# Kernel optimization log

Hardware: AMD Instinct MI355X
Metric: run time of the kernel (lower is better)

## Reference

```python
import jax, jax.numpy as jnp
import numpy as np

N_NODES = 100000


def gcn_conv(x, W, b, src, dst, num_nodes):
    # PyG GCNConv: add self-loops, symmetric normalization, x @ W, scatter-add, + b
    xw = x @ W  # [N, out]
    loop = jnp.arange(num_nodes, dtype=src.dtype)
    s = jnp.concatenate([src, loop])  # message source j
    d = jnp.concatenate([dst, loop])  # aggregation target i
    deg = jax.ops.segment_sum(jnp.ones_like(d, dtype=xw.dtype), d, num_segments=num_nodes)
    dis = jnp.where(deg > 0, jax.lax.rsqrt(deg), 0.0)  # D^{-1/2}
    norm = dis[s] * dis[d]  # [E+N]
    msg = norm[:, None] * xw[s]  # gather + scale
    out = jax.ops.segment_sum(msg, d, num_segments=num_nodes)  # scatter-add
    return out + b


def setup_inputs() -> dict:
    key = jax.random.key(0)
    k1, k2, k3, k4 = jax.random.split(key, 4)
    F, H, E = 64, 64, 1250000
    x = jax.random.normal(k1, (N_NODES, F), dtype=jnp.float32)
    edge_index = jax.random.randint(k2, (2, E), 0, N_NODES, dtype=jnp.int64)
    W1 = jax.random.normal(k3, (F, H), dtype=jnp.float32) * (1.0 / np.sqrt(F))
    b1 = jnp.zeros((H,), dtype=jnp.float32)
    W2 = jax.random.normal(k4, (H, F), dtype=jnp.float32) * (1.0 / np.sqrt(H))
    b2 = jnp.zeros((F,), dtype=jnp.float32)
    return {"x": x, "edge_index": edge_index, "W1": W1, "b1": b1, "W2": W2, "b2": b2}


def reference(x, edge_index, W1, b1, W2, b2):
    src, dst = edge_index[0], edge_index[1]
    h = gcn_conv(x, W1, b1, src, dst, N_NODES)
    h = jax.nn.relu(h)
    out = gcn_conv(h, W2, b2, src, dst, N_NODES)
    return out
```

## Files before the change

### kernel.cpp

```cpp
#include <hip/hip_runtime.h>

#define NN    100000
#define F     64
#define NBUCK 391
#define CAPB  4096
#define TILE  4096
#define NBLKG 782
#define G1A   400

#define O_CURSOR 0
#define O_ROWPTR 512
#define O_DEG    100864
#define O_DIS    201216
#define O_PACKED 301568
#define O_SRT    1903104
#define O_AH     3504768
#define O_BH     6704768
#define O_W2F    9904768

typedef __attribute__((ext_vector_type(8))) short bf16x8;
typedef __attribute__((ext_vector_type(4))) float f32x4;
typedef __attribute__((ext_vector_type(2))) float f32x2;

__device__ __forceinline__ unsigned bf_rne(float x) {
    unsigned u = __float_as_uint(x);
    return (u + 0x7FFFu + ((u >> 16) & 1u)) >> 16;
}
__device__ __forceinline__ unsigned pack2(float lo, float hi) {
    return bf_rne(lo) | (bf_rne(hi) << 16);
}
__device__ __forceinline__ float lo_f(unsigned u) { return __uint_as_float(u << 16); }
__device__ __forceinline__ float hi_f(unsigned u) { return __uint_as_float(u & 0xFFFF0000u); }
__device__ __forceinline__ f32x2 up2(unsigned u) {
    f32x2 r = {__uint_as_float(u << 16), __uint_as_float(u & 0xFFFF0000u)};
    return r;
}

struct BpSmem {
    int hist[NBUCK], lofs[NBUCK], gbase[NBUCK], lcur[NBUCK];
    int wsum[8];
    unsigned stage[TILE];
    unsigned short sbuck[TILE];
};
union KSmem {
    BpSmem bp;
    unsigned w1f[16][64][4];
};
struct NsSmem {
    int h[256], lcur[256], wsum[4], ptot;
    int stage[CAPB];
};
union K2Smem {
    NsSmem ns;
    unsigned w1f[16][64][4];
};
struct K3Smem {
    unsigned w2f[16][64][4];
    unsigned hbuf[16 * 32];
    float dis_s[16];
};

__device__ __forceinline__ void binpack_body(const int* __restrict__ src,
                                             const int* __restrict__ dst, int E,
                                             int* __restrict__ cursor,
                                             unsigned* __restrict__ packed,
                                             int bid, BpSmem& sm) {
    int t  = threadIdx.x;
    int t0 = bid * TILE;
    int n  = min(TILE, E - t0);

    if (t < NBUCK) sm.hist[t] = 0;
    __syncthreads();
    int d_r[8], s_r[8];
#pragma unroll
    for (int it = 0; it < 8; ++it) {
        int i = t + it * 512;
        if (i < n) {
            d_r[it] = dst[t0 + i];
            s_r[it] = src[t0 + i];
            atomicAdd(&sm.hist[d_r[it] >> 8], 1);
        }
    }
    __syncthreads();
    int lane = t & 63, w = t >> 6;
    int v = (t < NBUCK) ? sm.hist[t] : 0;
    int s = v;
#pragma unroll
    for (int off = 1; off < 64; off <<= 1) {
        int u = __shfl_up(s, off, 64);
        if (lane >= off) s += u;
    }
    if (lane == 63) sm.wsum[w] = s;
    __syncthreads();
    if (t == 0) {
        int run = 0;
#pragma unroll
        for (int i = 0; i < 8; ++i) { int c = sm.wsum[i]; sm.wsum[i] = run; run += c; }
    }
    __syncthreads();
    if (t < NBUCK) {
        int ex = s - v + sm.wsum[w];
        sm.lofs[t] = ex;
        sm.lcur[t] = ex;
        sm.gbase[t] = t * CAPB + (v ? atomicAdd(&cursor[t], v) : 0);
    }
    __syncthreads();
#pragma unroll
    for (int it = 0; it < 8; ++it) {
        int i = t + it * 512;
        if (i < n) {
            int d = d_r[it];
            int b = d >> 8;
            int p = atomicAdd(&sm.lcur[b], 1);
            sm.stage[p] = ((unsigned)s_r[it] << 8) | (unsigned)(d & 255);
            sm.sbuck[p] = (unsigned short)b;
        }
    }
    __syncthreads();
    for (int i = t; i < n; i += 512) {
        int b = sm.sbuck[i];
        packed[sm.gbase[b] + (i - sm.lofs[b])] = sm.stage[i];
    }
}

__device__ __forceinline__ void gemm_mfma_body(const float* __restrict__ X,
                                               const float* __restrict__ W,
                                               unsigned* __restrict__ Ah, int bid,
                                               unsigned (*w1f)[64][4]) {
    int t = threadIdx.x;
    for (int idx = t; idx < 4096; idx += 512) {
        int slot = idx >> 8;
        int ks   = (slot >> 1) & 1;
        int p    = slot & 1;
        int ct   = slot >> 2;
        int l    = (idx >> 2) & 63;
        int j    = idx & 3;
        int k    = 32 * ks + 8 * (l >> 4) + 2 * j;
        int col  = 16 * ct + (l & 15);
        float v0 = W[k * 64 + col];
        float v1 = W[(k + 1) * 64 + col];
        if (p) {
            v0 -= __uint_as_float(bf_rne(v0) << 16);
            v1 -= __uint_as_float(bf_rne(v1) << 16);
        }
        ((unsigned*)w1f)[idx] = pack2(v0, v1);
    }

    int lane = t & 63, wid = t >> 6;
    int g = lane >> 4;
    int wrow0 = bid * 128 + wid * 16;
    int wrow  = wrow0 + (lane & 15);
    bool valid = wrow < NN;
    const float* xp = X + (size_t)wrow * F + 8 * g;
    float4 fz = {0.f, 0.f, 0.f, 0.f};
    float4 f0 = valid ? *(const float4*)(xp)      : fz;
    float4 f1 = valid ? *(const float4*)(xp + 4)  : fz;
    float4 f2 = valid ? *(const float4*)(xp + 32) : fz;
    float4 f3 = valid ? *(const float4*)(xp + 36) : fz;
    __syncthreads();

    f32x4 ac0 = {0.f,0.f,0.f,0.f}, ac1 = ac0, ac2 = ac0, ac3 = ac0;
#pragma unroll
    for (int ks = 0; ks < 2; ++ks) {
        float4 u0 = ks ? f2 : f0;
        float4 u1 = ks ? f3 : f1;
        uint4 hw;
        hw.x = pack2(u0.x, u0.y);
        hw.y = pack2(u0.z, u0.w);
        hw.z = pack2(u1.x, u1.y);
        hw.w = pack2(u1.z, u1.w);
        uint4 lw;
        lw.x = pack2(u0.x - lo_f(hw.x), u0.y - hi_f(hw.x));
        lw.y = pack2(u0.z - lo_f(hw.y), u0.w - hi_f(hw.y));
        lw.z = pack2(u1.x - lo_f(hw.z), u1.y - hi_f(hw.z));
        lw.w = pack2(u1.z - lo_f(hw.w), u1.w - hi_f(hw.w));
        bf16x8 Ahi = __builtin_bit_cast(bf16x8, hw);
        bf16x8 Alo = __builtin_bit_cast(bf16x8, lw);
#pragma unroll
        for (int ct = 0; ct < 4; ++ct) {
            uint4 bh = *(const uint4*)&w1f[ct * 4 + ks * 2 + 0][lane][0];
            uint4 bl = *(const uint4*)&w1f[ct * 4 + ks * 2 + 1][lane][0];
            bf16x8 Bh_ = __builtin_bit_cast(bf16x8, bh);
            bf16x8 Bl_ = __builtin_bit_cast(bf16x8, bl);
            f32x4& ac = (ct == 0) ? ac0 : (ct == 1) ? ac1 : (ct == 2) ? ac2 : ac3;
            ac = __builtin_amdgcn_mfma_f32_16x16x32_bf16(Ahi, Bh_, ac, 0, 0, 0);
            ac = __builtin_amdgcn_mfma_f32_16x16x32_bf16(Alo, Bh_, ac, 0, 0, 0);
            ac = __builtin_amdgcn_mfma_f32_16x16x32_bf16(Ahi, Bl_, ac, 0, 0, 0);
        }
    }
#pragma unroll
    for (int ct = 0; ct < 4; ++ct) {
        f32x4 ac = (ct == 0) ? ac0 : (ct == 1) ? ac1 : (ct == 2) ? ac2 : ac3;
#pragma unroll
        for (int r = 0; r < 4; ++r) {
            float val = ac[r];
            float q = __shfl_xor(val, 1, 64);
            int row = wrow0 + 4 * g + r;
            if (!(lane & 1) && row < NN) {
                int colp = 8 * ct + ((lane & 15) >> 1);
                Ah[(size_t)row * 32 + colp] = pack2(val, q);
            }
        }
    }
}

__device__ __forceinline__ void w2prep_body(const float* __restrict__ W2,
                                            unsigned* __restrict__ w2f) {
    int t = threadIdx.x;
    for (int idx = t; idx < 4096; idx += 512) {
        int slot = idx >> 8;
        int ks   = (slot >> 1) & 1;
        int p    = slot & 1;
        int ct   = slot >> 2;
        int l    = (idx >> 2) & 63;
        int j    = idx & 3;
        int k    = 32 * ks + 8 * (l >> 4) + 2 * j;
        int col  = 16 * ct + (l & 15);
        float v0 = W2[k * 64 + col];
        float v1 = W2[(k + 1) * 64 + col];
        if (p) {
            v0 -= __uint_as_float(bf_rne(v0) << 16);
            v1 -= __uint_as_float(bf_rne(v1) << 16);
        }
        w2f[idx] = pack2(v0, v1);
    }
}

__device__ __forceinline__ void node_sort_body(const unsigned* __restrict__ packed,
                                               const int* __restrict__ cursor,
                                               int* __restrict__ row_ptr,
                                               int* __restrict__ deg,
                                               float* __restrict__ dis,
                                               int* __restrict__ srt,
                                               int b, NsSmem& sm) {
    int t = threadIdx.x;
    int nbase = b << 8;
    int nloc = min(256, NN - nbase);
    int beg = b * CAPB;
    int n = cursor[b];

    if (t < 256) sm.h[t] = 0;
    __syncthreads();
    unsigned p_r[8];
#pragma unroll
    for (int it = 0; it < 8; ++it) {
        int i = t + it * 512;
        if (i < n) {
            p_r[it] = packed[beg + i];
            atomicAdd(&sm.h[p_r[it] & 255u], 1);
        }
    }
    __syncthreads();
    int lane = t & 63, w = t >> 6;
    int v = 0, pd = 0, s = 0;
    if (t < 256) { v = sm.h[t]; pd = (v + 1) & ~1; s = pd; }
#pragma unroll
    for (int off = 1; off < 64; off <<= 1) {
        int u = __shfl_up(s, off, 64);
        if (lane >= off) s += u;
    }
    if (t < 256 && lane == 63) sm.wsum[w] = s;
    __syncthreads();
    if (t == 0) {
        int run = 0;
#pragma unroll
        for (int i = 0; i < 4; ++i) { int c = sm.wsum[i]; sm.wsum[i] = run; run += c; }
    }
    __syncthreads();
    if (t < 256) {
        int e0 = s - pd + sm.wsum[w];
        sm.lcur[t] = e0;
        if (t < nloc) {
            row_ptr[nbase + t] = beg + e0;
            deg[nbase + t]     = v;
            dis[nbase + t]     = rsqrtf((float)v + 1.0f);
        }
        if (t == nloc - 1) sm.ptot = e0 + pd;
    }
    __syncthreads();
#pragma unroll
    for (int it = 0; it < 8; ++it) {
        int i = t + it * 512;
        if (i < n) {
            unsigned p = p_r[it];
            int pos = atomicAdd(&sm.lcur[p & 255u], 1);
            sm.stage[pos] = (int)((p >> 8) << 7);
        }
    }
    __syncthreads();
    int ptot = sm.ptot;
    for (int i = t; i < ptot; i += 512) srt[beg + i] = sm.stage[i];
}

__global__ __launch_bounds__(512) void pre_gemm1(const int* __restrict__ src,
                                                 const int* __restrict__ dst, int E,
                                                 int nbp, int* __restrict__ cursor,
                                                 unsigned* __restrict__ packed,
                                                 const float* __restrict__ X,
                                                 const float* __restrict__ W1,
                                                 unsigned* __restrict__ Ah,
                                                 const float* __restrict__ W2,
                                                 unsigned* __restrict__ w2f) {
    __shared__ KSmem sm;
    if ((int)blockIdx.x < nbp)
        binpack_body(src, dst, E, cursor, packed, blockIdx.x, sm.bp);
    else if ((int)blockIdx.x < nbp + G1A)
        gemm_mfma_body(X, W1, Ah, (int)blockIdx.x - nbp, sm.w1f);
    else
        w2prep_body(W2, w2f);
}

__global__ __launch_bounds__(512) void sort_gemm1(const unsigned* __restrict__ packed,
                                                  const int* __restrict__ cursor,
                                                  int* __restrict__ row_ptr,
                                                  int* __restrict__ deg,
                                                  float* __restrict__ dis,
                                                  int* __restrict__ srt,
                                                  const float* __restrict__ X,
                                                  const float* __restrict__ W1,
                                                  unsigned* __restrict__ Ah) {
    __shared__ K2Smem sm;
    if ((int)blockIdx.x < NBUCK)
        node_sort_body(packed, cursor, row_ptr, deg, dis, srt, blockIdx.x, sm.ns);
    else
        gemm_mfma_body(X, W1, Ah, G1A + (int)blockIdx.x - NBUCK, sm.w1f);
}

__global__ __launch_bounds__(256) void agg1_gemm2(const unsigned* __restrict__ AhW,
                                                  const int* __restrict__ row_ptr,
                                                  const int* __restrict__ deg,
                                                  const int* __restrict__ srt,
                                                  const float* __restrict__ dis,
                                                  const float* __restrict__ b1,
                                                  const unsigned* __restrict__ w2fg,
                                                  unsigned* __restrict__ Bh) {
    __shared__ K3Smem sm;
    int t = threadIdx.x;
#pragma unroll
    for (int i = 0; i < 4; ++i)
        ((uint4*)sm.w2f)[t + 256 * i] = ((const uint4*)w2fg)[t + 256 * i];

    const char* baseA = (const char*)AhW;
    int sub  = t & 7;
    int grp  = (t >> 3) & 1;
    int soff = sub * 16;
    int node = blockIdx.x * 16 + (t >> 4);
    int cnt = deg[node];
    int beg = row_ptr[node];
    float di = dis[node];

    f32x2 A0, A1, A2, A3;
    if (grp == 0) {
        uint4 su = *(const uint4*)(baseA + ((size_t)node * 128 + soff));
        A0 = f32x2{di * lo_f(su.x), di * hi_f(su.x)};
        A1 = f32x2{di * lo_f(su.y), di * hi_f(su.y)};
        A2 = f32x2{di * lo_f(su.z), di * hi_f(su.z)};
        A3 = f32x2{di * lo_f(su.w), di * hi_f(su.w)};
    } else {
        A0 = A1 = A2 = A3 = f32x2{0.f, 0.f};
    }

    int h  = min(cnt, ((cnt >> 1) + 1) & ~1);
    int jb = beg + (grp ? h : 0);
    int je = jb + (grp ? (cnt - h) : h);
    for (; jb + 4 <= je; jb += 4) {
        int2 sa = *(const int2*)&srt[jb];
        int2 sb = *(const int2*)&srt[jb + 2];
        float d0 = dis[(unsigned)sa.x >> 7];
        float d1 = dis[(unsigned)sa.y >> 7];
        float d2 = dis[(unsigned)sb.x >> 7];
        float d3 = dis[(unsigned)sb.y >> 7];
        uint4 g0 = *(const uint4*)(baseA + (sa.x + soff));
        uint4 g1 = *(const uint4*)(baseA + (sa.y + soff));
        uint4 g2 = *(const uint4*)(baseA + (sb.x + soff));
        uint4 g3 = *(const uint4*)(baseA + (sb.y + soff));
        f32x2 dd0 = {d0, d0}, dd1 = {d1, d1}, dd2 = {d2, d2}, dd3 = {d3, d3};
        A0 = __builtin_elementwise_fma(dd0, up2(g0.x), A0);
        A1 = __builtin_elementwise_fma(dd0, up2(g0.y), A1);
        A2 = __builtin_elementwise_fma(dd0, up2(g0.z), A2);
        A3 = __builtin_elementwise_fma(dd0, up2(g0.w), A3);
        A0 = __builtin_elementwise_fma(dd1, up2(g1.x), A0);
        A1 = __builtin_elementwise_fma(dd1, up2(g1.y), A1);
        A2 = __builtin_elementwise_fma(dd1, up2(g1.z), A2);
        A3 = __builtin_elementwise_fma(dd1, up2(g1.w), A3);
        A0 = __builtin_elementwise_fma(dd2, up2(g2.x), A0);
        A1 = __builtin_elementwise_fma(dd2, up2(g2.y), A1);
        A2 = __builtin_elementwise_fma(dd2, up2(g2.z), A2);
        A3 = __builtin_elementwise_fma(dd2, up2(g2.w), A3);
        A0 = __builtin_elementwise_fma(dd3, up2(g3.x), A0);
        A1 = __builtin_elementwise_fma(dd3, up2(g3.y), A1);
        A2 = __builtin_elementwise_fma(dd3, up2(g3.z), A2);
        A3 = __builtin_elementwise_fma(dd3, up2(g3.w), A3);
    }
    for (; jb + 2 <= je; jb += 2) {
        int2 sa = *(const int2*)&srt[jb];
        float d0 = dis[(unsigned)sa.x >> 7];
        float d1 = dis[(unsigned)sa.y >> 7];
        uint4 g0 = *(const uint4*)(baseA + (sa.x + soff));
        uint4 g1 = *(const uint4*)(baseA + (sa.y + soff));
        f32x2 dd0 = {d0, d0}, dd1 = {d1, d1};
        A0 = __builtin_elementwise_fma(dd0, up2(g0.x), A0);
        A1 = __builtin_elementwise_fma(dd0, up2(g0.y), A1);
        A2 = __builtin_elementwise_fma(dd0, up2(g0.z), A2);
        A3 = __builtin_elementwise_fma(dd0, up2(g0.w), A3);
        A0 = __builtin_elementwise_fma(dd1, up2(g1.x), A0);
        A1 = __builtin_elementwise_fma(dd1, up2(g1.y), A1);
        A2 = __builtin_elementwise_fma(dd1, up2(g1.z), A2);
        A3 = __builtin_elementwise_fma(dd1, up2(g1.w), A3);
    }
    if (jb < je) {
        int sa = srt[jb];
        float d0 = dis[(unsigned)sa >> 7];
        uint4 g0 = *(const uint4*)(baseA + (sa + soff));
        f32x2 dd0 = {d0, d0};
        A0 = __builtin_elementwise_fma(dd0, up2(g0.x), A0);
        A1 = __builtin_elementwise_fma(dd0, up2(g0.y), A1);
        A2 = __builtin_elementwise_fma(dd0, up2(g0.z), A2);
        A3 = __builtin_elementwise_fma(dd0, up2(g0.w), A3);
    }
    float a0 = A0.x, a1 = A0.y, a2 = A1.x, a3 = A1.y;
    float a4 = A2.x, a5 = A2.y, a6 = A3.x, a7 = A3.y;
    a0 += __shfl_xor(a0, 8, 64); a1 += __shfl_xor(a1, 8, 64);
    a2 += __shfl_xor(a2, 8, 64); a3 += __shfl_xor(a3, 8, 64);
    a4 += __shfl_xor(a4, 8, 64); a5 += __shfl_xor(a5, 8, 64);
    a6 += __shfl_xor(a6, 8, 64); a7 += __shfl_xor(a7, 8, 64);

    float4 bb0 = ((const float4*)b1)[2 * sub];
    float4 bb1 = ((const float4*)b1)[2 * sub + 1];
    float o0 = fmaxf(fmaf(di, a0, bb0.x), 0.f);
    float o1 = fmaxf(fmaf(di, a1, bb0.y), 0.f);
    float o2 = fmaxf(fmaf(di, a2, bb0.z), 0.f);
    float o3 = fmaxf(fmaf(di, a3, bb0.w), 0.f);
    float o4 = fmaxf(fmaf(di, a4, bb1.x), 0.f);
    float o5 = fmaxf(fmaf(di, a5, bb1.y), 0.f);
    float o6 = fmaxf(fmaf(di, a6, bb1.z), 0.f);
    float o7 = fmaxf(fmaf(di, a7, bb1.w), 0.f);

    int node15 = t >> 4;
    if (!(t & 8)) {
        int unit = sub ^ (node15 & 7);
        uint4 hv;
        hv.x = pack2(o0, o1);
        hv.y = pack2(o2, o3);
        hv.z = pack2(o4, o5);
        hv.w = pack2(o6, o7);
        *(uint4*)&sm.hbuf[node15 * 32 + unit * 4] = hv;
        if (sub == 0) sm.dis_s[node15] = di;
    }
    __syncthreads();

    int lane = t & 63, ct = t >> 6;
    int row = lane & 15, g = lane >> 4;
    f32x4 acc = {0.f, 0.f, 0.f, 0.f};
#pragma unroll
    for (int ks = 0; ks < 2; ++ks) {
        int unit = (4 * ks + g) ^ (row & 7);
        uint4 araw = *(const uint4*)&sm.hbuf[row * 32 + unit * 4];
        uint4 bhr  = *(const uint4*)&sm.w2f[ct * 4 + ks * 2 + 0][lane][0];
        uint4 blr  = *(const uint4*)&sm.w2f[ct * 4 + ks * 2 + 1][lane][0];
        bf16x8 A  = __builtin_bit_cast(bf16x8, araw);
        bf16x8 Bh_ = __builtin_bit_cast(bf16x8, bhr);
        bf16x8 Bl_ = __builtin_bit_cast(bf16x8, blr);
        acc = __builtin_amdgcn_mfma_f32_16x16x32_bf16(A, Bh_, acc, 0, 0, 0);
        acc = __builtin_amdgcn_mfma_f32_16x16x32_bf16(A, Bl_, acc, 0, 0, 0);
    }
    int nbase16 = blockIdx.x * 16;
#pragma unroll
    for (int r = 0; r < 4; ++r) {
        int nd = 4 * g + r;
        float val = acc[r] * sm.dis_s[nd];
        float q = __shfl_xor(val, 1, 64);
        if (!(lane & 1)) {
            int colp = 8 * ct + ((lane & 15) >> 1);
            Bh[(size_t)(nbase16 + nd) * 32 + colp] = pack2(val, q);
        }
    }
}

__global__ __launch_bounds__(256) void agg_out(const unsigned* __restrict__ BsW,
                                               const int* __restrict__ row_ptr,
                                               const int* __restrict__ deg,
                                               const int* __restrict__ srt,
                                               const float* __restrict__ dis,
                                               const float* __restrict__ bias,
                                               float* __restrict__ outp) {
    int t = threadIdx.x;
    const char* baseB = (const char*)BsW;
    int sub  = t & 7;
    int grp  = (t >> 3) & 1;
    int soff = sub * 16;
    int node = blockIdx.x * 16 + (t >> 4);
    int cnt = deg[node];
    int beg = row_ptr[node];
    float di = dis[node];

    f32x2 A0, A1, A2, A3;
    if (grp == 0) {
        uint4 su = *(const uint4*)(baseB + ((size_t)node * 128 + soff));
        A0 = up2(su.x); A1 = up2(su.y); A2 = up2(su.z); A3 = up2(su.w);
    } else {
        A0 = A1 = A2 = A3 = f32x2{0.f, 0.f};
    }

    int h  = min(cnt, ((cnt >> 1) + 1) & ~1);
    int jb = beg + (grp ? h : 0);
    int je = jb + (grp ? (cnt - h) : h);
    for (; jb + 4 <= je; jb += 4) {
        int2 sa = *(const int2*)&srt[jb];
        int2 sb = *(const int2*)&srt[jb + 2];
        uint4 g0 = *(const uint4*)(baseB + (sa.x + soff));
        uint4 g1 = *(const uint4*)(baseB + (sa.y + soff));
        uint4 g2 = *(const uint4*)(baseB + (sb.x + soff));
        uint4 g3 = *(const uint4*)(baseB + (sb.y + soff));
        A0 = A0 + (up2(g0.x) + up2(g1.x)) + (up2(g2.x) + up2(g3.x));
        A1 = A1 + (up2(g0.y) + up2(g1.y)) + (up2(g2.y) + up2(g3.y));
        A2 = A2 + (up2(g0.z) + up2(g1.z)) + (up2(g2.z) + up2(g3.z));
        A3 = A3 + (up2(g0.w) + up2(g1.w)) + (up2(g2.w) + up2(g3.w));
    }
    for (; jb + 2 <= je; jb += 2) {
        int2 sa = *(const int2*)&srt[jb];
        uint4 g0 = *(const uint4*)(baseB + (sa.x + soff));
        uint4 g1 = *(const uint4*)(baseB + (sa.y + soff));
        A0 = A0 + up2(g0.x) + up2(g1.x);
        A1 = A1 + up2(g0.y) + up2(g1.y);
        A2 = A2 + up2(g0.z) + up2(g1.z);
        A3 = A3 + up2(g0.w) + up2(g1.w);
    }
    if (jb < je) {
        int sa = srt[jb];
        uint4 g0 = *(const uint4*)(baseB + (sa + soff));
        A0 = A0 + up2(g0.x);
        A1 = A1 + up2(g0.y);
        A2 = A2 + up2(g0.z);
        A3 = A3 + up2(g0.w);
    }
    float a0 = A0.x, a1 = A0.y, a2 = A1.x, a3 = A1.y;
    float a4 = A2.x, a5 = A2.y, a6 = A3.x, a7 = A3.y;
    a0 += __shfl_xor(a0, 8, 64); a1 += __shfl_xor(a1, 8, 64);
    a2 += __shfl_xor(a2, 8, 64); a3 += __shfl_xor(a3, 8, 64);
    a4 += __shfl_xor(a4, 8, 64); a5 += __shfl_xor(a5, 8, 64);
    a6 += __shfl_xor(a6, 8, 64); a7 += __shfl_xor(a7, 8, 64);

    float4 bb0 = ((const float4*)bias)[2 * sub];
    float4 bb1 = ((const float4*)bias)[2 * sub + 1];
    float4 o;
    if (grp == 0) {
        o.x = fmaf(di, a0, bb0.x);
        o.y = fmaf(di, a1, bb0.y);
        o.z = fmaf(di, a2, bb0.z);
        o.w = fmaf(di, a3, bb0.w);
        ((float4*)outp)[(size_t)node * 16 + 2 * sub] = o;
    } else {
        o.x = fmaf(di, a4, bb1.x);
        o.y = fmaf(di, a5, bb1.y);
        o.z = fmaf(di, a6, bb1.z);
        o.w = fmaf(di, a7, bb1.w);
        ((float4*)outp)[(size_t)node * 16 + 2 * sub + 1] = o;
    }
}

extern "C" void kernel_launch(void* const* d_in, const int* in_sizes, int n_in,
                              void* d_out, int out_size, void* d_ws, size_t ws_size,
                              hipStream_t stream) {
    const float* x  = (const float*)d_in[0];
    const int*   ei = (const int*)d_in[1];
    const float* W1 = (const float*)d_in[2];
    const float* b1 = (const float*)d_in[3];
    const float* W2 = (const float*)d_in[4];
    const float* b2 = (const float*)d_in[5];
    float* out = (float*)d_out;
    int E = in_sizes[1] / 2;
    const int* src = ei;
    const int* dst = ei + E;

    int*      ws_i    = (int*)d_ws;
    int*      cursor  = ws_i + O_CURSOR;
    int*      row_ptr = ws_i + O_ROWPTR;
    int*      deg     = ws_i + O_DEG;
    float*    dis     = (float*)(ws_i + O_DIS);
    unsigned* packed  = (unsigned*)(ws_i + O_PACKED);
    int*      srt     = ws_i + O_SRT;
    unsigned* Ah      = (unsigned*)(ws_i + O_AH);
    unsigned* Bh      = (unsigned*)(ws_i + O_BH);
    unsigned* w2f     = (unsigned*)(ws_i + O_W2F);

    int nbp = (E + TILE - 1) / TILE;

    (void)hipMemsetAsync(cursor, 0, NBUCK * sizeof(int), stream);
    pre_gemm1<<<nbp + G1A + 1, 512, 0, stream>>>(src, dst, E, nbp, cursor, packed,
                                                 x, W1, Ah, W2, w2f);
    sort_gemm1<<<NBUCK + (NBLKG - G1A), 512, 0, stream>>>(packed, cursor, row_ptr,
                                                          deg, dis, srt, x, W1, Ah);
    agg1_gemm2<<<NN / 16, 256, 0, stream>>>(Ah, row_ptr, deg, srt,
                                            dis, b1, w2f, Bh);
    agg_out<<<NN / 16, 256, 0, stream>>>(Bh, row_ptr, deg, srt,
                                         dis, b2, out);
}
```

Baseline: 181.2 us.

## Split layer-2 features into two column planes for cache-friendly gather

The layer-2 bf16 feature matrix is stored as two separate 32-column planes instead of one interleaved 64-column row, and the final aggregation kernel runs two passes of blocks, each gathering only one plane. Each plane is half the size, so the random neighbour gathers in each pass touch a smaller working set that fits L2/LLC better. The cost is doubled traversal of the CSR index arrays (row_ptr, deg, srt read twice) and an extra grid of blocks.

```diff
diff --git a/kernel.cpp b/kernel.cpp
--- a/kernel.cpp
+++ b/kernel.cpp
@@ -7,6 +7,7 @@
 #define TILE  4096
 #define NBLKG 782
 #define G1A   400
+#define PLW   1600000
 
 #define O_CURSOR 0
 #define O_ROWPTR 512
@@ -472,7 +473,8 @@
         float q = __shfl_xor(val, 1, 64);
         if (!(lane & 1)) {
             int colp = 8 * ct + ((lane & 15) >> 1);
-            Bh[(size_t)(nbase16 + nd) * 32 + colp] = pack2(val, q);
+            int pl = colp >> 4, wd = colp & 15;
+            Bh[(size_t)pl * PLW + (size_t)(nbase16 + nd) * 16 + wd] = pack2(val, q);
         }
     }
 }
@@ -485,18 +487,20 @@
                                                const float* __restrict__ bias,
                                                float* __restrict__ outp) {
     int t = threadIdx.x;
-    const char* baseB = (const char*)BsW;
-    int sub  = t & 7;
-    int grp  = (t >> 3) & 1;
+    int half = (int)blockIdx.x >= 3125;
+    int nb   = (int)blockIdx.x - (half ? 3125 : 0);
+    const char* baseB = (const char*)(BsW + (size_t)half * PLW);
+    int sub  = t & 3;
+    int grp  = (t >> 2) & 1;
     int soff = sub * 16;
-    int node = blockIdx.x * 16 + (t >> 4);
+    int node = nb * 32 + (t >> 3);
     int cnt = deg[node];
     int beg = row_ptr[node];
     float di = dis[node];
 
     f32x2 A0, A1, A2, A3;
     if (grp == 0) {
-        uint4 su = *(const uint4*)(baseB + ((size_t)node * 128 + soff));
+        uint4 su = *(const uint4*)(baseB + ((size_t)node * 64 + soff));
         A0 = up2(su.x); A1 = up2(su.y); A2 = up2(su.z); A3 = up2(su.w);
     } else {
         A0 = A1 = A2 = A3 = f32x2{0.f, 0.f};
@@ -508,10 +512,10 @@
     for (; jb + 4 <= je; jb += 4) {
         int2 sa = *(const int2*)&srt[jb];
         int2 sb = *(const int2*)&srt[jb + 2];
-        uint4 g0 = *(const uint4*)(baseB + (sa.x + soff));
-        uint4 g1 = *(const uint4*)(baseB + (sa.y + soff));
-        uint4 g2 = *(const uint4*)(baseB + (sb.x + soff));
-        uint4 g3 = *(const uint4*)(baseB + (sb.y + soff));
+        uint4 g0 = *(const uint4*)(baseB + ((sa.x >> 1) + soff));
+        uint4 g1 = *(const uint4*)(baseB + ((sa.y >> 1) + soff));
+        uint4 g2 = *(const uint4*)(baseB + ((sb.x >> 1) + soff));
+        uint4 g3 = *(const uint4*)(baseB + ((sb.y >> 1) + soff));
         A0 = A0 + (up2(g0.x) + up2(g1.x)) + (up2(g2.x) + up2(g3.x));
         A1 = A1 + (up2(g0.y) + up2(g1.y)) + (up2(g2.y) + up2(g3.y));
         A2 = A2 + (up2(g0.z) + up2(g1.z)) + (up2(g2.z) + up2(g3.z));
@@ -519,8 +523,8 @@
     }
     for (; jb + 2 <= je; jb += 2) {
         int2 sa = *(const int2*)&srt[jb];
-        uint4 g0 = *(const uint4*)(baseB + (sa.x + soff));
-        uint4 g1 = *(const uint4*)(baseB + (sa.y + soff));
+        uint4 g0 = *(const uint4*)(baseB + ((sa.x >> 1) + soff));
+        uint4 g1 = *(const uint4*)(baseB + ((sa.y >> 1) + soff));
         A0 = A0 + up2(g0.x) + up2(g1.x);
         A1 = A1 + up2(g0.y) + up2(g1.y);
         A2 = A2 + up2(g0.z) + up2(g1.z);
@@ -528,7 +532,7 @@
     }
     if (jb < je) {
         int sa = srt[jb];
-        uint4 g0 = *(const uint4*)(baseB + (sa + soff));
+        uint4 g0 = *(const uint4*)(baseB + ((sa >> 1) + soff));
         A0 = A0 + up2(g0.x);
         A1 = A1 + up2(g0.y);
         A2 = A2 + up2(g0.z);
@@ -536,26 +540,26 @@
     }
     float a0 = A0.x, a1 = A0.y, a2 = A1.x, a3 = A1.y;
     float a4 = A2.x, a5 = A2.y, a6 = A3.x, a7 = A3.y;
-    a0 += __shfl_xor(a0, 8, 64); a1 += __shfl_xor(a1, 8, 64);
-    a2 += __shfl_xor(a2, 8, 64); a3 += __shfl_xor(a3, 8, 64);
-    a4 += __shfl_xor(a4, 8, 64); a5 += __shfl_xor(a5, 8, 64);
-    a6 += __shfl_xor(a6, 8, 64); a7 += __shfl_xor(a7, 8, 64);
-
-    float4 bb0 = ((const float4*)bias)[2 * sub];
-    float4 bb1 = ((const float4*)bias)[2 * sub + 1];
+    a0 += __shfl_xor(a0, 4, 64); a1 += __shfl_xor(a1, 4, 64);
+    a2 += __shfl_xor(a2, 4, 64); a3 += __shfl_xor(a3, 4, 64);
+    a4 += __shfl_xor(a4, 4, 64); a5 += __shfl_xor(a5, 4, 64);
+    a6 += __shfl_xor(a6, 4, 64); a7 += __shfl_xor(a7, 4, 64);
+
+    float4 bb0 = ((const float4*)bias)[8 * half + 2 * sub];
+    float4 bb1 = ((const float4*)bias)[8 * half + 2 * sub + 1];
     float4 o;
     if (grp == 0) {
         o.x = fmaf(di, a0, bb0.x);
         o.y = fmaf(di, a1, bb0.y);
         o.z = fmaf(di, a2, bb0.z);
         o.w = fmaf(di, a3, bb0.w);
-        ((float4*)outp)[(size_t)node * 16 + 2 * sub] = o;
+        ((float4*)outp)[(size_t)node * 16 + 8 * half + 2 * sub] = o;
     } else {
         o.x = fmaf(di, a4, bb1.x);
         o.y = fmaf(di, a5, bb1.y);
         o.z = fmaf(di, a6, bb1.z);
         o.w = fmaf(di, a7, bb1.w);
-        ((float4*)outp)[(size_t)node * 16 + 2 * sub + 1] = o;
+        ((float4*)outp)[(size_t)node * 16 + 8 * half + 2 * sub + 1] = o;
     }
 }
 
@@ -593,6 +597,6 @@
                                                           deg, dis, srt, x, W1, Ah);
     agg1_gemm2<<<NN / 16, 256, 0, stream>>>(Ah, row_ptr, deg, srt,
                                             dis, b1, w2f, Bh);
-    agg_out<<<NN / 16, 256, 0, stream>>>(Bh, row_ptr, deg, srt,
-                                         dis, b2, out);
-}
+    agg_out<<<2 * 3125, 256, 0, stream>>>(Bh, row_ptr, deg, srt,
+                                          dis, b2, out);
+}
```

Result: slower. 186.3 us (+2.9%).
